# Optimization experiments

Measured on AMD Instinct MI355X. Metric: run time of the kernel, lower is better.

The kernel has to match this reference:

```python
import jax, jax.numpy as jnp
import numpy as np

B, N, D = 2, 2048, 1024   # batch, seq_len, d_model
E = 2 * D                  # d_inner = d_model * expand_factor
F = 4 * D                  # ffn hidden
CHUNK = 128
EPS_LN = 1e-5


def setup_inputs() -> dict:
    key = jax.random.key(0)
    ks = jax.random.split(key, 16)
    s = 0.02
    return {
        "x": jax.random.normal(ks[0], (B, N, D), dtype=jnp.float32),
        # linear-attention projections (stored [in, out])
        "q_w": jax.random.normal(ks[1], (D, E), dtype=jnp.float32) * s,
        "q_b": jnp.zeros((E,), jnp.float32),
        "k_w": jax.random.normal(ks[2], (D, E), dtype=jnp.float32) * s,
        "k_b": jnp.zeros((E,), jnp.float32),
        "v_w": jax.random.normal(ks[3], (D, E), dtype=jnp.float32) * s,
        "v_b": jnp.zeros((E,), jnp.float32),
        "o_w": jax.random.normal(ks[4], (E, D), dtype=jnp.float32) * s,
        "o_b": jnp.zeros((D,), jnp.float32),
        # layer norms
        "ln1_g": jnp.ones((D,), jnp.float32), "ln1_b": jnp.zeros((D,), jnp.float32),
        "ln2_g": jnp.ones((D,), jnp.float32), "ln2_b": jnp.zeros((D,), jnp.float32),
        # ffn
        "w1": jax.random.normal(ks[5], (D, F), dtype=jnp.float32) * s,
        "b1": jnp.zeros((F,), jnp.float32),
        "w2": jax.random.normal(ks[6], (F, D), dtype=jnp.float32) * s,
        "b2": jnp.zeros((D,), jnp.float32),
    }


def _layer_norm(x, g, b):
    mu = jnp.mean(x, axis=-1, keepdims=True)
    var = jnp.mean(jnp.square(x - mu), axis=-1, keepdims=True)
    return (x - mu) * jax.lax.rsqrt(var + EPS_LN) * g + b


def _feature_map(x):
    return jax.nn.elu(x) + 1.0  # positive features


def _causal_linear_attention(Q, K, V):
    """Exactly cumsum(k v^T) formulation, computed chunk-recurrently.
    Q,K: [B,N,E] (post feature map), V: [B,N,E]. Returns [B,N,E]."""
    nC = N // CHUNK
    Qc = Q.reshape(B, nC, CHUNK, E).transpose(1, 0, 2, 3)
    Kc = K.reshape(B, nC, CHUNK, E).transpose(1, 0, 2, 3)
    Vc = V.reshape(B, nC, CHUNK, E).transpose(1, 0, 2, 3)
    tril = jnp.tril(jnp.ones((CHUNK, CHUNK), Q.dtype))

    def step(S, qkv):  # S: [B,E,E] running sum of k v^T
        q, k, v = qkv
        scores = jnp.einsum('bcd,bkd->bck', q, k) * tril  # intra-chunk causal
        intra = jnp.einsum('bck,bke->bce', scores, v)
        inter = jnp.einsum('bcd,bde->bce', q, S)
        S = S + jnp.einsum('bcd,bce->bde', k, v)
        return S, intra + inter

    S0 = jnp.zeros((B, E, E), Q.dtype)
    _, num = jax.lax.scan(step, S0, (Qc, Kc, Vc))  # [nC,B,CHUNK,E]
    num = num.transpose(1, 0, 2, 3).reshape(B, N, E)
    Z = jnp.cumsum(K, axis=1)                       # [B,N,E]
    den = jnp.einsum('bnd,bnd->bn', Q, Z)[..., None] + 1e-6
    return num / den


def reference(x, q_w, q_b, k_w, k_b, v_w, v_b, o_w, o_b,
              ln1_g, ln1_b, ln2_g, ln2_b, w1, b1, w2, b2):
    # training branch of SSDFLUIDLayer (linear attention), dropout = identity (eval)
    xn = _layer_norm(x, ln1_g, ln1_b)
    Q = _feature_map(xn @ q_w + q_b)
    K = _feature_map(xn @ k_w + k_b)
    V = xn @ v_w + v_b
    attn = _causal_linear_attention(Q, K, V) @ o_w + o_b
    x = x + attn
    xn2 = _layer_norm(x, ln2_g, ln2_b)
    ffn = jax.nn.gelu(xn2 @ w1 + b1, approximate=False) @ w2 + b2
    return x + ffn
```

## Files before the change

kernel.cpp:

```cpp
#include <hip/hip_runtime.h>
#include <math.h>

typedef unsigned short u16;
typedef short s16x8 __attribute__((ext_vector_type(8)));
typedef float f32x4 __attribute__((ext_vector_type(4)));
typedef long long ll;

__device__ inline u16 f2bf(float f) {
    unsigned u = __float_as_uint(f);
    u += 0x7fffu + ((u >> 16) & 1u);
    return (u16)(u >> 16);
}
__device__ inline float bf2f(u16 h) { return __uint_as_float(((unsigned)h) << 16); }

__device__ __forceinline__ void glds16(const u16* g, u16* l) {
    __builtin_amdgcn_global_load_lds(
        (__attribute__((address_space(1))) void*)(void*)g,
        (__attribute__((address_space(3))) void*)l, 16, 0, 0);
}

__global__ __launch_bounds__(256) void ln_bf16(const float* __restrict__ x,
                                               const float* __restrict__ g,
                                               const float* __restrict__ b,
                                               u16* __restrict__ out, int D) {
    int row = blockIdx.x;
    const float* xr = x + (size_t)row * D;
    int t = threadIdx.x;
    float4 v = ((const float4*)xr)[t];
    float s = v.x + v.y + v.z + v.w;
    __shared__ float sm[4];
    #pragma unroll
    for (int o = 32; o > 0; o >>= 1) s += __shfl_down(s, o, 64);
    int lane = t & 63, wv = t >> 6;
    if (lane == 0) sm[wv] = s;
    __syncthreads();
    float mean = (sm[0] + sm[1] + sm[2] + sm[3]) * (1.0f / 1024.0f);
    float dx = v.x - mean, dy = v.y - mean, dz = v.z - mean, dw = v.w - mean;
    float s2 = dx * dx + dy * dy + dz * dz + dw * dw;
    __syncthreads();
    #pragma unroll
    for (int o = 32; o > 0; o >>= 1) s2 += __shfl_down(s2, o, 64);
    if (lane == 0) sm[wv] = s2;
    __syncthreads();
    float var = (sm[0] + sm[1] + sm[2] + sm[3]) * (1.0f / 1024.0f);
    float rstd = rsqrtf(var + 1e-5f);
    float4 gg = ((const float4*)g)[t], bb = ((const float4*)b)[t];
    ushort4 o4;
    o4.x = f2bf(dx * rstd * gg.x + bb.x);
    o4.y = f2bf(dy * rstd * gg.y + bb.y);
    o4.z = f2bf(dz * rstd * gg.z + bb.z);
    o4.w = f2bf(dw * rstd * gg.w + bb.w);
    ((ushort4*)(out + (size_t)row * D))[t] = o4;
}

__global__ __launch_bounds__(256) void combine_ln(
    const float* __restrict__ x, const float* __restrict__ p0,
    const float* __restrict__ p1, const float* __restrict__ ob,
    const float* __restrict__ g, const float* __restrict__ b,
    float* __restrict__ x2, u16* __restrict__ xn2) {
    int row = blockIdx.x;
    int t = threadIdx.x;
    size_t base = (size_t)row * 256;
    float4 v = ((const float4*)x)[base + t];
    float4 a0 = ((const float4*)p0)[base + t];
    float4 a1 = ((const float4*)p1)[base + t];
    float4 ob4 = ((const float4*)ob)[t];
    v.x += a0.x + a1.x + ob4.x;
    v.y += a0.y + a1.y + ob4.y;
    v.z += a0.z + a1.z + ob4.z;
    v.w += a0.w + a1.w + ob4.w;
    ((float4*)x2)[base + t] = v;
    float s = v.x + v.y + v.z + v.w;
    __shared__ float sm[4];
    #pragma unroll
    for (int o = 32; o > 0; o >>= 1) s += __shfl_down(s, o, 64);
    int lane = t & 63, wv = t >> 6;
    if (lane == 0) sm[wv] = s;
    __syncthreads();
    float mean = (sm[0] + sm[1] + sm[2] + sm[3]) * (1.0f / 1024.0f);
    float dx = v.x - mean, dy = v.y - mean, dz = v.z - mean, dw = v.w - mean;
    float s2 = dx * dx + dy * dy + dz * dz + dw * dw;
    __syncthreads();
    #pragma unroll
    for (int o = 32; o > 0; o >>= 1) s2 += __shfl_down(s2, o, 64);
    if (lane == 0) sm[wv] = s2;
    __syncthreads();
    float var = (sm[0] + sm[1] + sm[2] + sm[3]) * (1.0f / 1024.0f);
    float rstd = rsqrtf(var + 1e-5f);
    float4 gg = ((const float4*)g)[t], bb = ((const float4*)b)[t];
    ushort4 o4;
    o4.x = f2bf(dx * rstd * gg.x + bb.x);
    o4.y = f2bf(dy * rstd * gg.y + bb.y);
    o4.z = f2bf(dz * rstd * gg.z + bb.z);
    o4.w = f2bf(dw * rstd * gg.w + bb.w);
    ((ushort4*)(xn2 + (size_t)row * 1024))[t] = o4;
}

__global__ __launch_bounds__(256) void combine_out(
    const float* __restrict__ x2, const float* __restrict__ p0,
    const float* __restrict__ p1, const float* __restrict__ b2,
    float* __restrict__ out) {
    size_t i = (size_t)blockIdx.x * 256 + threadIdx.x;
    int col4 = (int)(i & 255);
    float4 v = ((const float4*)x2)[i];
    float4 a0 = ((const float4*)p0)[i];
    float4 a1 = ((const float4*)p1)[i];
    float4 bb = ((const float4*)b2)[col4];
    v.x += a0.x + a1.x + bb.x;
    v.y += a0.y + a1.y + bb.y;
    v.z += a0.z + a1.z + bb.z;
    v.w += a0.w + a1.w + bb.w;
    ((float4*)out)[i] = v;
}

__global__ void prep(const float* __restrict__ qb, const float* __restrict__ kb,
                     const float* __restrict__ vb, float* __restrict__ bcat,
                     float* __restrict__ den, int E, int BN) {
    int i = blockIdx.x * 256 + threadIdx.x;
    if (i < E) {
        bcat[i] = qb[i];
        bcat[E + i] = kb[i];
        bcat[2 * E + i] = vb[i];
    }
    if (i < BN) den[i] = 0.f;
}

__global__ __launch_bounds__(256) void transpose_qkv(const float* __restrict__ s0,
                                                     const float* __restrict__ s1,
                                                     const float* __restrict__ s2,
                                                     u16* __restrict__ out, int R, int C) {
    int z = blockIdx.z;
    const float* in = (z == 0) ? s0 : (z == 1) ? s1 : s2;
    out += (size_t)z * C * R;
    __shared__ u16 tile[32][33];
    int tx = threadIdx.x & 31, ty = threadIdx.x >> 5;
    int c0 = blockIdx.x * 32, r0 = blockIdx.y * 32;
    #pragma unroll
    for (int i = 0; i < 32; i += 8)
        tile[ty + i][tx] = f2bf(in[(size_t)(r0 + ty + i) * C + c0 + tx]);
    __syncthreads();
    #pragma unroll
    for (int i = 0; i < 32; i += 8)
        out[(size_t)(c0 + ty + i) * R + r0 + tx] = tile[tx][ty + i];
}

template <typename Tin>
__global__ __launch_bounds__(256) void transpose_bf16(const Tin* __restrict__ in,
                                                      u16* __restrict__ out,
                                                      int R, int C, int ldIn,
                                                      ll sIn, ll sOut) {
    in += (size_t)blockIdx.z * sIn;
    out += (size_t)blockIdx.z * sOut;
    __shared__ u16 tile[32][33];
    int tx = threadIdx.x & 31, ty = threadIdx.x >> 5;
    int c0 = blockIdx.x * 32, r0 = blockIdx.y * 32;
    #pragma unroll
    for (int i = 0; i < 32; i += 8) {
        Tin v = in[(size_t)(r0 + ty + i) * ldIn + c0 + tx];
        if constexpr (sizeof(Tin) == 4) tile[ty + i][tx] = f2bf((float)v);
        else                            tile[ty + i][tx] = (u16)v;
    }
    __syncthreads();
    #pragma unroll
    for (int i = 0; i < 32; i += 8)
        out[(size_t)(c0 + ty + i) * R + r0 + tx] = tile[tx][ty + i];
}

enum { EPI_QKV = 0, EPI_TRIL = 2, EPI_DIV = 3, EPI_GELU = 5, EPI_PART = 6 };

#define TM 128
#define TN 128
#define BK 64

template <int EPI>
__global__ __launch_bounds__(256) void gemm_nt(
    const u16* __restrict__ A, const u16* __restrict__ B, void* __restrict__ Cv,
    const float* __restrict__ bias, float* __restrict__ den,
    int M, int N, int K, int lda, int ldb, int triK,
    ll sA, ll sB, ll sC, ll sAux) {
    int z = blockIdx.z;
    A += (size_t)z * sA;
    B += (size_t)z * sB;

    int nb = gridDim.x;
    int bl = blockIdx.y * nb + blockIdx.x;
    int panel = nb * 4;
    int pp = bl / panel, rr = bl - pp * panel;
    int m0 = (pp * 4 + (rr & 3)) * TM;
    int n0 = (rr >> 2) * TN;

    int t = threadIdx.x;

    if (EPI == EPI_TRIL && n0 > m0 + (TM - 1)) return;

    __shared__ __align__(16) u16 As[TM * BK];
    __shared__ __align__(16) u16 Bs[TN * BK];

    f32x4 acc[4][4];
    #pragma unroll
    for (int i = 0; i < 4; i++)
        #pragma unroll
        for (int j = 0; j < 4; j++) { f32x4 zz = {0.f, 0.f, 0.f, 0.f}; acc[i][j] = zz; }

    int kend = (EPI == EPI_DIV && triK) ? (m0 + TM < K ? m0 + TM : K) : K;

    int lane = t & 63, wv = t >> 6;
    int lr = lane & 15, q = lane >> 4;
    int wm = (wv & 1) * 64, wn = (wv >> 1) * 64;

    int srow = wv * 32 + (lane >> 3);
    int skf = (lane & 7) * 8;
    const u16* gA = A + (size_t)(m0 + srow) * lda + skf;
    const u16* gB = B + (size_t)(n0 + srow) * ldb + skf;
    u16* lA = As + wv * 32 * BK;
    u16* lB = Bs + wv * 32 * BK;

    for (int k0 = 0; k0 < kend; k0 += BK) {
        #pragma unroll
        for (int r = 0; r < 4; ++r) {
            glds16(gA + k0 + (size_t)(8 * r) * lda, lA + r * 8 * BK);
            glds16(gB + k0 + (size_t)(8 * r) * ldb, lB + r * 8 * BK);
        }
        __syncthreads();
        #pragma unroll
        for (int kk = 0; kk < 2; ++kk) {
            s16x8 af[4], bfr[4];
            #pragma unroll
            for (int i = 0; i < 4; i++)
                af[i] = *(const s16x8*)&As[(wm + i * 16 + lr) * BK + kk * 32 + q * 8];
            #pragma unroll
            for (int j = 0; j < 4; j++)
                bfr[j] = *(const s16x8*)&Bs[(wn + j * 16 + lr) * BK + kk * 32 + q * 8];
            #pragma unroll
            for (int i = 0; i < 4; i++)
                #pragma unroll
                for (int j = 0; j < 4; j++)
                    acc[i][j] = __builtin_amdgcn_mfma_f32_16x16x32_bf16(af[i], bfr[j], acc[i][j], 0, 0, 0);
        }
        __syncthreads();
    }

    u16* Cb = (u16*)Cv + (size_t)z * sC;
    float* Cf = (float*)Cv + (size_t)z * sC;
    bool isQK = (EPI == EPI_QKV) && (n0 < 4096);
    #pragma unroll
    for (int i = 0; i < 4; i++) {
        #pragma unroll
        for (int r = 0; r < 4; r++) {
            int row = m0 + wm + i * 16 + q * 4 + r;
            float rs = 0.f;
            #pragma unroll
            for (int j = 0; j < 4; j++) {
                int col = n0 + wn + j * 16 + lr;
                float v = acc[i][j][r];
                if (EPI == EPI_QKV) {
                    v += bias[col];
                    if (isQK) v = (v > 0.f) ? (v + 1.f) : __expf(v);
                    Cb[(size_t)row * N + col] = f2bf(v);
                } else if (EPI == EPI_TRIL) {
                    v = (col <= row) ? v : 0.f;
                    rs += v;
                    Cb[(size_t)row * N + col] = f2bf(v);
                } else if (EPI == EPI_DIV) {
                    float d = den[(size_t)z * sAux + row] + 1e-6f;
                    Cb[(size_t)row * N + col] = f2bf(v / d);
                } else if (EPI == EPI_GELU) {
                    v += bias[col];
                    float u = v * (0.7978845608f + 0.0356774081f * v * v);
                    u = fminf(u, 40.f);
                    float e = __expf(2.f * u);
                    v = v * __fdividef(e, e + 1.f);
                    Cb[(size_t)row * N + col] = f2bf(v);
                } else if (EPI == EPI_PART) {
                    Cf[(size_t)row * N + col] = v;
                }
            }
            if (EPI == EPI_TRIL) {
                #pragma unroll
                for (int m = 1; m < 16; m <<= 1) rs += __shfl_xor(rs, m, 16);
                if (lr == 0) atomicAdd(&den[(size_t)z * sAux + row], rs);
            }
        }
    }
}

extern "C" void kernel_launch(void* const* d_in, const int* in_sizes, int n_in,
                              void* d_out, int out_size, void* d_ws, size_t ws_size,
                              hipStream_t stream) {
    const float* x    = (const float*)d_in[0];
    const float* q_w  = (const float*)d_in[1];
    const float* q_b  = (const float*)d_in[2];
    const float* k_w  = (const float*)d_in[3];
    const float* k_b  = (const float*)d_in[4];
    const float* v_w  = (const float*)d_in[5];
    const float* v_b  = (const float*)d_in[6];
    const float* o_w  = (const float*)d_in[7];
    const float* o_b  = (const float*)d_in[8];
    const float* ln1g = (const float*)d_in[9];
    const float* ln1b = (const float*)d_in[10];
    const float* ln2g = (const float*)d_in[11];
    const float* ln2b = (const float*)d_in[12];
    const float* w1   = (const float*)d_in[13];
    const float* b1   = (const float*)d_in[14];
    const float* w2   = (const float*)d_in[15];
    const float* b2   = (const float*)d_in[16];
    float* out = (float*)d_out;

    constexpr int Bb = 2, N = 2048, D = 1024, E = 2048, F = 4096;
    constexpr int BN = Bb * N;
    constexpr int E3 = 3 * E;

    char* ws = (char*)d_ws;
    size_t off = 0;
    auto alloc = [&](size_t bytes) -> void* {
        void* p = ws + off;
        off += (bytes + 255) & ~(size_t)255;
        return p;
    };
    u16*   qkvT = (u16*)alloc((size_t)E3 * D * 2);
    u16*   oT   = (u16*)alloc((size_t)D * E * 2);
    u16*   w1T  = (u16*)alloc((size_t)F * D * 2);
    u16*   w2T  = (u16*)alloc((size_t)D * F * 2);
    float* bcat = (float*)alloc((size_t)E3 * 4);
    u16*   xn   = (u16*)alloc((size_t)BN * D * 2);
    u16*   QKV  = (u16*)alloc((size_t)BN * E3 * 2);
    u16*   Vt   = (u16*)alloc((size_t)Bb * E * N * 2);
    u16*   Amat = (u16*)alloc((size_t)Bb * N * N * 2);
    float* den  = (float*)alloc((size_t)BN * 4);

    u16*   xn2 = xn;
    u16*   P   = QKV;
    u16*   h   = QKV + (size_t)8 * 1024 * 1024;
    float* x2  = (float*)Vt;
    float* pt0 = (float*)Amat;
    float* pt1 = pt0 + (size_t)BN * D;

    dim3 blk(256);

    prep<<<dim3((BN + 255) / 256), blk, 0, stream>>>(q_b, k_b, v_b, bcat, den, E, BN);

    transpose_qkv<<<dim3(E / 32, D / 32, 3), blk, 0, stream>>>(q_w, k_w, v_w, qkvT, D, E);
    transpose_bf16<float><<<dim3(D / 32, E / 32, 1), blk, 0, stream>>>(o_w, oT, E, D, D, 0, 0);
    transpose_bf16<float><<<dim3(F / 32, D / 32, 1), blk, 0, stream>>>(w1, w1T, D, F, F, 0, 0);
    transpose_bf16<float><<<dim3(D / 32, F / 32, 1), blk, 0, stream>>>(w2, w2T, F, D, D, 0, 0);

    ln_bf16<<<BN, blk, 0, stream>>>(x, ln1g, ln1b, xn, D);

    gemm_nt<EPI_QKV><<<dim3(E3 / 128, BN / 128, 1), blk, 0, stream>>>(
        xn, qkvT, QKV, bcat, nullptr, BN, E3, D, D, D, 0, 0, 0, 0, 0);

    transpose_bf16<u16><<<dim3(E / 32, N / 32, Bb), blk, 0, stream>>>(
        QKV + 2 * E, Vt, N, E, E3, (ll)N * E3, (ll)E * N);

    gemm_nt<EPI_TRIL><<<dim3(N / 128, N / 128, Bb), blk, 0, stream>>>(
        QKV, QKV + E, Amat, nullptr, den, N, N, E, E3, E3, 0,
        (ll)N * E3, (ll)N * E3, (ll)N * N, (ll)N);

    gemm_nt<EPI_DIV><<<dim3(E / 128, N / 128, Bb), blk, 0, stream>>>(
        Amat, Vt, P, nullptr, den, N, E, N, N, N, 1,
        (ll)N * N, (ll)E * N, (ll)N * E, (ll)N);

    gemm_nt<EPI_PART><<<dim3(D / 128, BN / 128, 2), blk, 0, stream>>>(
        P, oT, pt0, nullptr, nullptr, BN, D, E / 2, E, E, 0,
        (ll)(E / 2), (ll)(E / 2), (ll)BN * D, 0);

    combine_ln<<<BN, blk, 0, stream>>>(x, pt0, pt1, o_b, ln2g, ln2b, x2, xn2);

    gemm_nt<EPI_GELU><<<dim3(F / 128, BN / 128, 1), blk, 0, stream>>>(
        xn2, w1T, h, b1, nullptr, BN, F, D, D, D, 0, 0, 0, 0, 0);

    gemm_nt<EPI_PART><<<dim3(D / 128, BN / 128, 2), blk, 0, stream>>>(
        h, w2T, pt0, nullptr, nullptr, BN, D, F / 2, F, F, 0,
        (ll)(F / 2), (ll)(F / 2), (ll)BN * D, 0);

    combine_out<<<dim3(BN * D / 4 / 256), blk, 0, stream>>>(x2, pt0, pt1, b2, out);
}
```

Measured before the change: 511.0 us.

## Halve GEMM K-tile and swizzle LDS layout to avoid bank conflicts

Reduces the K tile from 64 to 32 and reorganizes the global-to-LDS load so each row's 16-byte k-chunks are stored at rotated positions. Fragment reads use matching swizzled offsets, so lanes in a quad hit different banks. This aims to cut LDS bank conflicts in the MFMA fragment loads, at the cost of twice as many loop iterations and barriers per tile.

```diff
diff --git a/kernel.cpp b/kernel.cpp
--- a/kernel.cpp
+++ b/kernel.cpp
@@ -170,7 +170,7 @@
 
 #define TM 128
 #define TN 128
-#define BK 64
+#define BK 32
 
 template <int EPI>
 __global__ __launch_bounds__(256) void gemm_nt(
@@ -208,35 +208,41 @@
     int lr = lane & 15, q = lane >> 4;
     int wm = (wv & 1) * 64, wn = (wv >> 1) * 64;
 
-    int srow = wv * 32 + (lane >> 3);
-    int skf = (lane & 7) * 8;
-    const u16* gA = A + (size_t)(m0 + srow) * lda + skf;
-    const u16* gB = B + (size_t)(n0 + srow) * ldb + skf;
+    int srow = wv * 32 + (lane >> 2);
+    int sq = ((lane & 3) - ((lane >> 3) & 3)) & 3;
+    int skf = sq * 8;
+    const u16* gA0 = A + (size_t)(m0 + srow) * lda + skf;
+    const u16* gA1 = gA0 + (size_t)16 * lda;
+    const u16* gB0 = B + (size_t)(n0 + srow) * ldb + skf;
+    const u16* gB1 = gB0 + (size_t)16 * ldb;
     u16* lA = As + wv * 32 * BK;
     u16* lB = Bs + wv * 32 * BK;
 
+    int ca[4], cb[4];
+    #pragma unroll
+    for (int i = 0; i < 4; i++) {
+        int ra = wm + i * 16 + lr;
+        ca[i] = (ra * 4 + ((q + (ra >> 1)) & 3)) * 8;
+        int rb = wn + i * 16 + lr;
+        cb[i] = (rb * 4 + ((q + (rb >> 1)) & 3)) * 8;
+    }
+
     for (int k0 = 0; k0 < kend; k0 += BK) {
-        #pragma unroll
-        for (int r = 0; r < 4; ++r) {
-            glds16(gA + k0 + (size_t)(8 * r) * lda, lA + r * 8 * BK);
-            glds16(gB + k0 + (size_t)(8 * r) * ldb, lB + r * 8 * BK);
-        }
+        glds16(gA0 + k0, lA);
+        glds16(gA1 + k0, lA + 16 * BK);
+        glds16(gB0 + k0, lB);
+        glds16(gB1 + k0, lB + 16 * BK);
         __syncthreads();
-        #pragma unroll
-        for (int kk = 0; kk < 2; ++kk) {
-            s16x8 af[4], bfr[4];
-            #pragma unroll
-            for (int i = 0; i < 4; i++)
-                af[i] = *(const s16x8*)&As[(wm + i * 16 + lr) * BK + kk * 32 + q * 8];
+        s16x8 af[4], bfr[4];
+        #pragma unroll
+        for (int i = 0; i < 4; i++) af[i] = *(const s16x8*)&As[ca[i]];
+        #pragma unroll
+        for (int j = 0; j < 4; j++) bfr[j] = *(const s16x8*)&Bs[cb[j]];
+        #pragma unroll
+        for (int i = 0; i < 4; i++)
             #pragma unroll
             for (int j = 0; j < 4; j++)
-                bfr[j] = *(const s16x8*)&Bs[(wn + j * 16 + lr) * BK + kk * 32 + q * 8];
-            #pragma unroll
-            for (int i = 0; i < 4; i++)
-                #pragma unroll
-                for (int j = 0; j < 4; j++)
-                    acc[i][j] = __builtin_amdgcn_mfma_f32_16x16x32_bf16(af[i], bfr[j], acc[i][j], 0, 0, 0);
-        }
+                acc[i][j] = __builtin_amdgcn_mfma_f32_16x16x32_bf16(af[i], bfr[j], acc[i][j], 0, 0, 0);
         __syncthreads();
     }
 
```

New measurement: 522.8 us. 1.02x slower.
